# Kernel tuning notes

Measured on AMD Instinct MI355X. Metric: run time of the kernel, lower is better.

## Reference

```python
import jax, jax.numpy as jnp
import numpy as np
from jax import lax

E, L, S, F = 4, 8, 512, 32
SAMPLE_SIZE = 512
BATCH_LEN = 64
TRAIN_ENVS = [0, 1, 2]


def setup_inputs() -> dict:
    key = jax.random.key(0)
    k1, k2 = jax.random.split(key)
    data_len = jax.random.randint(k2, (E, L), S // 2, S + 1).astype(jnp.int32)
    matrix = jax.random.normal(k1, (E, L, S, F), dtype=jnp.float32)
    # zero-pad samples beyond each (env,label) length, as shape_to_matrix does
    mask = (jnp.arange(S)[None, None, :, None] < data_len[:, :, None, None])
    matrix = matrix * mask.astype(jnp.float32)
    params = jnp.eye(F, dtype=jnp.float32)
    return {"matrix": matrix, "params": params, "data_len": data_len}


def _pair_indices():
    train_idx, test_idx = [], []
    for i in range(E):
        for j in range(E):
            idx = i * E + j
            if i < j:
                test_idx.append(idx)
                if i in TRAIN_ENVS and j in TRAIN_ENVS:
                    train_idx.append(idx)
    return np.array(train_idx), np.array(test_idx)


def reference(matrix, params, data_len):
    # normalize by mean per-(env,label,feature) std (torch.std is unbiased -> ddof=1)
    std = jnp.std(matrix, axis=2, ddof=1).mean()
    m = matrix / std
    bw = 1.06 * (S ** (-1.0 / 5.0)) * jnp.std(m, axis=2, ddof=1).mean()
    lenf = data_len.astype(jnp.float32)                     # [E,L]
    proj = jnp.einsum('elsf,fg->elsg', m, params)           # [E,L,S,F]

    left = lax.stop_gradient(proj.min())
    right = lax.stop_gradient(proj.max())
    delta = (right - left) / SAMPLE_SIZE
    grid = jnp.linspace(left, right, SAMPLE_SIZE)           # [G]
    divisor = jnp.sqrt(2.0 * jnp.pi) * bw

    n_chunks = SAMPLE_SIZE // BATCH_LEN
    grid_chunks = grid.reshape(n_chunks, BATCH_LEN)
    inv2bw2 = 0.5 / (bw * bw)
    pad_count = (float(S) - lenf)[:, :, None, None]         # [E,L,1,1]
    lend = lenf[:, :, None, None]

    def step(carry, pts):
        # Gaussian KDE kernel: offset^(d^2) == exp(-0.5*d^2/bw^2)
        d2 = (proj[..., None] - pts) ** 2                   # [E,L,S,F,C]
        ksum = jnp.exp(-inv2bw2 * d2).sum(axis=2)           # [E,L,F,C]
        corr = pad_count * jnp.exp(-inv2bw2 * pts ** 2)     # zero-padding correction
        red = (ksum - corr) / lend                          # [E,L,F,C]
        diff = jnp.abs(red[:, None] - red[None, :]).sum(-1) # [E,E,L,F]
        return carry + diff, None

    store, _ = lax.scan(step, jnp.zeros((E, E, L, F), dtype=proj.dtype), grid_chunks)
    store_dis = (store / divisor).reshape(E * E, L, F)

    train_idx, test_idx = _pair_indices()
    test_results = (store_dis[test_idx] * delta / 2.0).max(axis=0)    # [L,F]
    train_results = (store_dis[train_idx] * delta / 2.0).max(axis=0)  # [L,F]
    train_dis = train_results.max(axis=0).mean()
    test_dis = test_results.max(axis=0).mean()
    return train_results, test_results, train_dis, test_dis
```

## Files before the change

### kernel.cpp

```cpp
#include <hip/hip_runtime.h>
#include <float.h>


#if __has_builtin(__builtin_amdgcn_exp2f)
__device__ __forceinline__ float fast_exp2(float x) { return __builtin_amdgcn_exp2f(x); }
#else
__device__ __forceinline__ float fast_exp2(float x) { return exp2f(x); }
#endif

#define PT_OFF    0
#define SX_OFF    524288
#define SXX_OFF   532480
#define MIN_OFF   540672
#define MAX_OFF   540928
#define CNT_OFF   541184

__global__ __launch_bounds__(256) void stage_prep(const float* __restrict__ matrix,
                                                  const float* __restrict__ params,
                                                  float* __restrict__ PT,
                                                  float* __restrict__ sxg,
                                                  float* __restrict__ sxxg,
                                                  float* __restrict__ minp,
                                                  float* __restrict__ maxp,
                                                  int* __restrict__ counter) {
    __shared__ float M[64][33];
    __shared__ float Pm[32][32];
    __shared__ float sxr[8][32], sxxr[8][32];
    __shared__ float rmin[4], rmax[4];
    const int bid = blockIdx.x;
    const int s0 = (bid & 7) << 6;
    const int el = bid >> 3;
    const int t = threadIdx.x;
    if (bid == 0 && t == 0) *counter = 0;
    {
        const float4 v = reinterpret_cast<const float4*>(params)[t];
        const int base = t << 2;
        Pm[base >> 5][base & 31]       = v.x;
        Pm[base >> 5][(base & 31) + 1] = v.y;
        Pm[base >> 5][(base & 31) + 2] = v.z;
        Pm[base >> 5][(base & 31) + 3] = v.w;
    }
    const float4* mb4 = reinterpret_cast<const float4*>(matrix + (size_t)(el * 512 + s0) * 32);
    #pragma unroll
    for (int k = t; k < 512; k += 256) {
        const float4 v = mb4[k];
        const int base = k << 2;
        M[base >> 5][base & 31]       = v.x;
        M[base >> 5][(base & 31) + 1] = v.y;
        M[base >> 5][(base & 31) + 2] = v.z;
        M[base >> 5][(base & 31) + 3] = v.w;
    }
    __syncthreads();
    {
        const int f = t & 31, r = t >> 5;
        float sx = 0.f, sxx = 0.f;
        #pragma unroll
        for (int k = 0; k < 8; ++k) {
            float v = M[r * 8 + k][f];
            sx += v; sxx += v * v;
        }
        sxr[r][f] = sx; sxxr[r][f] = sxx;
    }
    const int s = t & 63;
    const int g0 = t >> 6;
    float lmin = FLT_MAX, lmax = -FLT_MAX;
    #pragma unroll
    for (int pass = 0; pass < 8; ++pass) {
        const int g = (pass << 2) + g0;
        float acc = 0.f;
        #pragma unroll
        for (int fp = 0; fp < 32; ++fp) acc += M[s][fp] * Pm[fp][g];
        lmin = fminf(lmin, acc);
        lmax = fmaxf(lmax, acc);
        PT[(size_t)(el * 32 + g) * 512 + s0 + s] = acc;
    }
    #pragma unroll
    for (int off = 32; off >= 1; off >>= 1) {
        lmin = fminf(lmin, __shfl_xor(lmin, off, 64));
        lmax = fmaxf(lmax, __shfl_xor(lmax, off, 64));
    }
    if ((t & 63) == 0) { rmin[t >> 6] = lmin; rmax[t >> 6] = lmax; }
    __syncthreads();
    if (t < 32) {
        float a = 0.f, b = 0.f;
        #pragma unroll
        for (int r = 0; r < 8; ++r) { a += sxr[r][t]; b += sxxr[r][t]; }
        sxg[bid * 32 + t] = a;
        sxxg[bid * 32 + t] = b;
    }
    if (t == 0) {
        minp[bid] = fminf(fminf(rmin[0], rmin[1]), fminf(rmin[2], rmin[3]));
        maxp[bid] = fmaxf(fmaxf(rmax[0], rmax[1]), fmaxf(rmax[2], rmax[3]));
    }
}

__global__ __launch_bounds__(1024, 4) void stage_kde2(const float* __restrict__ PT,
                                                      const float* __restrict__ sxg,
                                                      const float* __restrict__ sxxg,
                                                      const float* __restrict__ minp,
                                                      const float* __restrict__ maxp,
                                                      const int* __restrict__ dlen,
                                                      int* __restrict__ counter,
                                                      float* __restrict__ out) {
    __shared__ __align__(16) float xs[4][512];
    __shared__ float red[4][512];
    __shared__ float wsum[16], wmn[16], wmx[16];
    __shared__ float wred[8][6];
    __shared__ float csh[6];
    __shared__ int lastf;
    const int t = threadIdx.x;
    const int lf = blockIdx.x;
    const int l = lf >> 5, f = lf & 31;

    {
        const int el = t >> 5, fc = t & 31;
        const int base = el * 256 + fc;
        float Sx = 0.f, Sxx = 0.f;
        #pragma unroll
        for (int tile = 0; tile < 8; ++tile) { Sx += sxg[base + tile * 32]; Sxx += sxxg[base + tile * 32]; }
        const float mean = Sx * (1.0f / 512.0f);
        const float var = (Sxx - Sx * mean) * (1.0f / 511.0f);
        float sf = sqrtf(fmaxf(var, 0.f));
        float mn = (t < 256) ? minp[t] : FLT_MAX;
        float mx = (t < 256) ? maxp[t] : -FLT_MAX;
        #pragma unroll
        for (int off = 32; off >= 1; off >>= 1) {
            sf += __shfl_xor(sf, off, 64);
            mn = fminf(mn, __shfl_xor(mn, off, 64));
            mx = fmaxf(mx, __shfl_xor(mx, off, 64));
        }
        if ((t & 63) == 0) { wsum[t >> 6] = sf; wmn[t >> 6] = mn; wmx[t >> 6] = mx; }
        __syncthreads();
        if (t == 0) {
            float s = 0.f, lo = FLT_MAX, hi = -FLT_MAX;
            #pragma unroll
            for (int w = 0; w < 16; ++w) {
                s += wsum[w]; lo = fminf(lo, wmn[w]); hi = fmaxf(hi, wmx[w]);
            }
            const float stdv = s * (1.0f / 1024.0f);
            const float left  = lo / stdv;
            const float right = hi / stdv;
            const float bw = 1.06f * 0.28717458874925877f;
            const float delta = (right - left) * (1.0f / 512.0f);
            const float gstep = (right - left) * (1.0f / 511.0f);
            const float divisor = 2.5066282746310002f * bw;
            const float cpos = (0.5f / (bw * bw)) * 1.4426950408889634f;
            const float kf = sqrtf(cpos);
            csh[0] = left;
            csh[1] = gstep;
            csh[2] = kf;
            csh[3] = (1.0f / stdv) * kf;
            csh[4] = delta * 0.5f / divisor;
        }
    }
    __syncthreads();
    const float left = csh[0], gstep = csh[1], kf = csh[2], xscale = csh[3];

    #pragma unroll
    for (int k = t; k < 2048; k += 1024) {
        const int e2 = k >> 9, s2 = k & 511;
        xs[e2][s2] = PT[((size_t)(((e2 << 3) + l) * 32 + f) << 9) + s2] * xscale;
    }
    __syncthreads();

    const int h = t >> 9, g = t & 511;
    const float p = fmaf((float)g, gstep, left) * kf;
    #pragma unroll
    for (int ei = 0; ei < 2; ++ei) {
        const int e = (h << 1) + ei;
        const int len = dlen[(e << 3) + l];
        const float* __restrict__ x = xs[e];
        float a0 = 0.f, a1 = 0.f, a2 = 0.f, a3 = 0.f;
        float a4 = 0.f, a5 = 0.f, a6 = 0.f, a7 = 0.f;
        int s = 0;
        for (; s + 8 <= len; s += 8) {
            const float4 v0 = *reinterpret_cast<const float4*>(&x[s]);
            const float4 v1 = *reinterpret_cast<const float4*>(&x[s + 4]);
            const float d0 = v0.x - p, d1 = v0.y - p, d2 = v0.z - p, d3 = v0.w - p;
            const float d4 = v1.x - p, d5 = v1.y - p, d6 = v1.z - p, d7 = v1.w - p;
            a0 += fast_exp2(-(d0 * d0));
            a1 += fast_exp2(-(d1 * d1));
            a2 += fast_exp2(-(d2 * d2));
            a3 += fast_exp2(-(d3 * d3));
            a4 += fast_exp2(-(d4 * d4));
            a5 += fast_exp2(-(d5 * d5));
            a6 += fast_exp2(-(d6 * d6));
            a7 += fast_exp2(-(d7 * d7));
        }
        for (; s < len; ++s) {
            const float d = x[s] - p;
            a0 += fast_exp2(-(d * d));
        }
        red[e][g] = (((a0 + a1) + (a2 + a3)) + ((a4 + a5) + (a6 + a7))) / (float)len;
    }
    __syncthreads();

    if (t < 512) {
        const float r0 = red[0][t], r1 = red[1][t], r2 = red[2][t], r3 = red[3][t];
        float pr[6];
        pr[0] = fabsf(r0 - r1);
        pr[1] = fabsf(r0 - r2);
        pr[2] = fabsf(r0 - r3);
        pr[3] = fabsf(r1 - r2);
        pr[4] = fabsf(r1 - r3);
        pr[5] = fabsf(r2 - r3);
        #pragma unroll
        for (int pi = 0; pi < 6; ++pi) {
            float v = pr[pi];
            #pragma unroll
            for (int off = 32; off >= 1; off >>= 1) v += __shfl_xor(v, off, 64);
            if ((t & 63) == 0) wred[t >> 6][pi] = v;
        }
    }
    __syncthreads();
    if (t == 0) {
        const float scale = csh[4];
        float v[6];
        #pragma unroll
        for (int pi = 0; pi < 6; ++pi) {
            float sm = 0.f;
            #pragma unroll
            for (int w = 0; w < 8; ++w) sm += wred[w][pi];
            v[pi] = sm * scale;
        }
        float testv = v[0];
        #pragma unroll
        for (int pi = 1; pi < 6; ++pi) testv = fmaxf(testv, v[pi]);
        const float trainv = fmaxf(fmaxf(v[0], v[1]), v[3]);
        out[lf] = trainv;
        out[256 + lf] = testv;
        __threadfence();
        const int old = __hip_atomic_fetch_add(counter, 1, __ATOMIC_ACQ_REL,
                                               __HIP_MEMORY_SCOPE_AGENT);
        lastf = (old == 255);
    }
    __syncthreads();

    if (lastf && t < 64) {
        const int ff = t & 31;
        const int base = (t >= 32) ? 256 : 0;
        float m = -FLT_MAX;
        #pragma unroll
        for (int ll = 0; ll < 8; ++ll) {
            const float val = __hip_atomic_load(&out[base + ll * 32 + ff],
                                                __ATOMIC_RELAXED, __HIP_MEMORY_SCOPE_AGENT);
            m = fmaxf(m, val);
        }
        #pragma unroll
        for (int off = 16; off >= 1; off >>= 1) m += __shfl_xor(m, off, 32);
        if (ff == 0) out[512 + (base ? 1 : 0)] = m * (1.0f / 32.0f);
    }
}

extern "C" void kernel_launch(void* const* d_in, const int* in_sizes, int n_in,
                              void* d_out, int out_size, void* d_ws, size_t ws_size,
                              hipStream_t stream) {
    (void)in_sizes; (void)n_in; (void)out_size; (void)ws_size;
    const float* matrix = (const float*)d_in[0];
    const float* params = (const float*)d_in[1];
    const int*   dlen   = (const int*)d_in[2];
    float* out = (float*)d_out;
    float* ws  = (float*)d_ws;
    float* PT   = ws + PT_OFF;
    float* sxg  = ws + SX_OFF;
    float* sxxg = ws + SXX_OFF;
    float* minp = ws + MIN_OFF;
    float* maxp = ws + MAX_OFF;
    int*   cnt  = (int*)(ws + CNT_OFF);

    hipLaunchKernelGGL(stage_prep, dim3(256), dim3(256), 0, stream,
                       matrix, params, PT, sxg, sxxg, minp, maxp, cnt);
    hipLaunchKernelGGL(stage_kde2, dim3(256), dim3(1024), 0, stream,
                       PT, sxg, sxxg, minp, maxp, dlen, cnt, out);
}
```

Baseline: 102.1 us.

## Halve KDE block size and register-block four grid points per thread

Measured after the change: 101.6 us. No clear change (-0.6%).

```diff
diff --git a/kernel.cpp b/kernel.cpp
--- a/kernel.cpp
+++ b/kernel.cpp
@@ -94,17 +94,17 @@
     }
 }
 
-__global__ __launch_bounds__(1024, 4) void stage_kde2(const float* __restrict__ PT,
-                                                      const float* __restrict__ sxg,
-                                                      const float* __restrict__ sxxg,
-                                                      const float* __restrict__ minp,
-                                                      const float* __restrict__ maxp,
-                                                      const int* __restrict__ dlen,
-                                                      int* __restrict__ counter,
-                                                      float* __restrict__ out) {
+__global__ __launch_bounds__(512) void stage_kde2(const float* __restrict__ PT,
+                                                  const float* __restrict__ sxg,
+                                                  const float* __restrict__ sxxg,
+                                                  const float* __restrict__ minp,
+                                                  const float* __restrict__ maxp,
+                                                  const int* __restrict__ dlen,
+                                                  int* __restrict__ counter,
+                                                  float* __restrict__ out) {
     __shared__ __align__(16) float xs[4][512];
     __shared__ float red[4][512];
-    __shared__ float wsum[16], wmn[16], wmx[16];
+    __shared__ float wsum[8], wmn[8], wmx[8];
     __shared__ float wred[8][6];
     __shared__ float csh[6];
     __shared__ int lastf;
@@ -113,14 +113,18 @@
     const int l = lf >> 5, f = lf & 31;
 
     {
-        const int el = t >> 5, fc = t & 31;
-        const int base = el * 256 + fc;
-        float Sx = 0.f, Sxx = 0.f;
-        #pragma unroll
-        for (int tile = 0; tile < 8; ++tile) { Sx += sxg[base + tile * 32]; Sxx += sxxg[base + tile * 32]; }
-        const float mean = Sx * (1.0f / 512.0f);
-        const float var = (Sxx - Sx * mean) * (1.0f / 511.0f);
-        float sf = sqrtf(fmaxf(var, 0.f));
+        float sf = 0.f;
+        #pragma unroll
+        for (int tr = t; tr < 1024; tr += 512) {
+            const int el = tr >> 5, fc = tr & 31;
+            const int base = el * 256 + fc;
+            float Sx = 0.f, Sxx = 0.f;
+            #pragma unroll
+            for (int tile = 0; tile < 8; ++tile) { Sx += sxg[base + tile * 32]; Sxx += sxxg[base + tile * 32]; }
+            const float mean = Sx * (1.0f / 512.0f);
+            const float var = (Sxx - Sx * mean) * (1.0f / 511.0f);
+            sf += sqrtf(fmaxf(var, 0.f));
+        }
         float mn = (t < 256) ? minp[t] : FLT_MAX;
         float mx = (t < 256) ? maxp[t] : -FLT_MAX;
         #pragma unroll
@@ -134,7 +138,7 @@
         if (t == 0) {
             float s = 0.f, lo = FLT_MAX, hi = -FLT_MAX;
             #pragma unroll
-            for (int w = 0; w < 16; ++w) {
+            for (int w = 0; w < 8; ++w) {
                 s += wsum[w]; lo = fminf(lo, wmn[w]); hi = fmaxf(hi, wmx[w]);
             }
             const float stdv = s * (1.0f / 1024.0f);
@@ -157,45 +161,65 @@
     const float left = csh[0], gstep = csh[1], kf = csh[2], xscale = csh[3];
 
     #pragma unroll
-    for (int k = t; k < 2048; k += 1024) {
+    for (int k = t; k < 2048; k += 512) {
         const int e2 = k >> 9, s2 = k & 511;
         xs[e2][s2] = PT[((size_t)(((e2 << 3) + l) * 32 + f) << 9) + s2] * xscale;
     }
     __syncthreads();
 
-    const int h = t >> 9, g = t & 511;
-    const float p = fmaf((float)g, gstep, left) * kf;
-    #pragma unroll
-    for (int ei = 0; ei < 2; ++ei) {
-        const int e = (h << 1) + ei;
-        const int len = dlen[(e << 3) + l];
-        const float* __restrict__ x = xs[e];
-        float a0 = 0.f, a1 = 0.f, a2 = 0.f, a3 = 0.f;
-        float a4 = 0.f, a5 = 0.f, a6 = 0.f, a7 = 0.f;
-        int s = 0;
-        for (; s + 8 <= len; s += 8) {
-            const float4 v0 = *reinterpret_cast<const float4*>(&x[s]);
-            const float4 v1 = *reinterpret_cast<const float4*>(&x[s + 4]);
-            const float d0 = v0.x - p, d1 = v0.y - p, d2 = v0.z - p, d3 = v0.w - p;
-            const float d4 = v1.x - p, d5 = v1.y - p, d6 = v1.z - p, d7 = v1.w - p;
-            a0 += fast_exp2(-(d0 * d0));
-            a1 += fast_exp2(-(d1 * d1));
-            a2 += fast_exp2(-(d2 * d2));
-            a3 += fast_exp2(-(d3 * d3));
-            a4 += fast_exp2(-(d4 * d4));
-            a5 += fast_exp2(-(d5 * d5));
-            a6 += fast_exp2(-(d6 * d6));
-            a7 += fast_exp2(-(d7 * d7));
-        }
-        for (; s < len; ++s) {
-            const float d = x[s] - p;
-            a0 += fast_exp2(-(d * d));
-        }
-        red[e][g] = (((a0 + a1) + (a2 + a3)) + ((a4 + a5) + (a6 + a7))) / (float)len;
-    }
-    __syncthreads();
-
-    if (t < 512) {
+    const int e = t >> 7, gl = t & 127;
+    const int len = dlen[(e << 3) + l];
+    float p[4];
+    #pragma unroll
+    for (int j = 0; j < 4; ++j)
+        p[j] = fmaf((float)(gl + 128 * j), gstep, left) * kf;
+    const float* __restrict__ x = xs[e];
+    float acc[4][2];
+    #pragma unroll
+    for (int j = 0; j < 4; ++j) { acc[j][0] = 0.f; acc[j][1] = 0.f; }
+    const int len4 = len & ~3;
+    int s = 0;
+    if (len4 > 0) {
+        float4 v = *reinterpret_cast<const float4*>(&x[0]);
+        for (s = 4; s < len4; s += 4) {
+            const float4 nv = *reinterpret_cast<const float4*>(&x[s]);
+            #pragma unroll
+            for (int j = 0; j < 4; ++j) {
+                const float d0 = v.x - p[j], d1 = v.y - p[j];
+                const float d2 = v.z - p[j], d3 = v.w - p[j];
+                acc[j][0] += fast_exp2(-(d0 * d0));
+                acc[j][1] += fast_exp2(-(d1 * d1));
+                acc[j][0] += fast_exp2(-(d2 * d2));
+                acc[j][1] += fast_exp2(-(d3 * d3));
+            }
+            v = nv;
+        }
+        #pragma unroll
+        for (int j = 0; j < 4; ++j) {
+            const float d0 = v.x - p[j], d1 = v.y - p[j];
+            const float d2 = v.z - p[j], d3 = v.w - p[j];
+            acc[j][0] += fast_exp2(-(d0 * d0));
+            acc[j][1] += fast_exp2(-(d1 * d1));
+            acc[j][0] += fast_exp2(-(d2 * d2));
+            acc[j][1] += fast_exp2(-(d3 * d3));
+        }
+        s = len4;
+    }
+    for (; s < len; ++s) {
+        const float xv = x[s];
+        #pragma unroll
+        for (int j = 0; j < 4; ++j) {
+            const float d = xv - p[j];
+            acc[j][0] += fast_exp2(-(d * d));
+        }
+    }
+    const float inv_len = 1.0f / (float)len;
+    #pragma unroll
+    for (int j = 0; j < 4; ++j)
+        red[e][gl + 128 * j] = (acc[j][0] + acc[j][1]) * inv_len;
+    __syncthreads();
+
+    {
         const float r0 = red[0][t], r1 = red[1][t], r2 = red[2][t], r3 = red[3][t];
         float pr[6];
         pr[0] = fabsf(r0 - r1);
@@ -270,6 +294,6 @@
 
     hipLaunchKernelGGL(stage_prep, dim3(256), dim3(256), 0, stream,
                        matrix, params, PT, sxg, sxxg, minp, maxp, cnt);
-    hipLaunchKernelGGL(stage_kde2, dim3(256), dim3(1024), 0, stream,
+    hipLaunchKernelGGL(stage_kde2, dim3(256), dim3(512), 0, stream,
                        PT, sxg, sxxg, minp, maxp, dlen, cnt, out);
 }
```
